# Kernel optimization log

Hardware: AMD Instinct MI355X
Metric: run time of the kernel (lower is better)

The kernel has to match this reference:

```python
import jax, jax.numpy as jnp
import numpy as np

B, FREQ, FRAMES = 16, 513, 2048
N_FFT, HOP, WIN = 1024, 256, 1024


def _hann_periodic(n):
    # torch.hann_window(n) (periodic): 0.5 - 0.5*cos(2*pi*k/n)
    return (0.5 - 0.5 * jnp.cos(2.0 * jnp.pi * jnp.arange(n) / n)).astype(jnp.float32)


def setup_inputs() -> dict:
    key = jax.random.key(0)
    k1, k2 = jax.random.split(key)
    spec_real = jax.random.normal(k1, (B, FREQ, FRAMES), dtype=jnp.float32)
    spec_imag = jax.random.normal(k2, (B, FREQ, FRAMES), dtype=jnp.float32)
    window = _hann_periodic(WIN)
    return {
        "spec_real": spec_real,
        "spec_imag": spec_imag,
        "window": window,
        "n_fft": N_FFT,
        "hop_length": HOP,
        "win_length": WIN,
    }


def reference(spec_real, spec_imag, window, n_fft, hop_length, win_length):
    spec = spec_real + 1j * spec_imag          # [B, n_fft//2+1, n_frames] complex
    n_frames = spec.shape[-1]
    pad = (win_length - hop_length) // 2
    # irfft with torch norm='backward' == jnp default norm
    ifft = jnp.fft.irfft(spec, n=n_fft, axis=1)           # [B, n_fft, F]
    frames = (ifft * window[None, :, None]).transpose(0, 2, 1)
    out_len = (n_frames - 1) * hop_length + win_length
    # overlap-add (fold) via scatter-add
    idx = jnp.arange(n_frames)[:, None] * hop_length + jnp.arange(win_length)[None, :]
    audio = jnp.zeros((frames.shape[0], out_len), frames.dtype).at[:, idx].add(frames)
    # squared-window envelope via the same overlap-add
    env = jnp.zeros((out_len,), window.dtype).at[idx].add(
        jnp.broadcast_to(window * window, (n_frames, win_length))
    )
    audio = audio[:, pad:out_len - pad] / env[pad:out_len - pad]
    return audio[:, None, :]  # [B, 1, T]
```

## Files before the change

### kernel.cpp

```cpp
#include <hip/hip_runtime.h>


#define B_      16
#define FREQ_   513
#define FRAMES_ 2048
#define NFFT_   1024
#define HOP_    256
#define NH_     512
#define PAD_    384
#define T_OUT_  524288
#define HPW     12
#define SPW     3072
#define NCHUNK  171

#define ZSTR2   513
#define XWSTR   513
#define TWF     16416
#define PREF    17440
#define LDSF    18464

__device__ __forceinline__ void idft8(float* zr, float* zi) {
  const float C = 0.70710678118654752f;
  float tr, ti;
  tr = zr[0]-zr[4]; ti = zi[0]-zi[4]; zr[0]+=zr[4]; zi[0]+=zi[4]; zr[4]=tr;         zi[4]=ti;
  tr = zr[1]-zr[5]; ti = zi[1]-zi[5]; zr[1]+=zr[5]; zi[1]+=zi[5]; zr[5]=C*(tr-ti);  zi[5]=C*(tr+ti);
  tr = zr[2]-zr[6]; ti = zi[2]-zi[6]; zr[2]+=zr[6]; zi[2]+=zi[6]; zr[6]=-ti;        zi[6]=tr;
  tr = zr[3]-zr[7]; ti = zi[3]-zi[7]; zr[3]+=zr[7]; zi[3]+=zi[7]; zr[7]=-C*(tr+ti); zi[7]=C*(tr-ti);
  tr = zr[0]-zr[2]; ti = zi[0]-zi[2]; zr[0]+=zr[2]; zi[0]+=zi[2]; zr[2]=tr;  zi[2]=ti;
  tr = zr[1]-zr[3]; ti = zi[1]-zi[3]; zr[1]+=zr[3]; zi[1]+=zi[3]; zr[3]=-ti; zi[3]=tr;
  tr = zr[4]-zr[6]; ti = zi[4]-zi[6]; zr[4]+=zr[6]; zi[4]+=zi[6]; zr[6]=tr;  zi[6]=ti;
  tr = zr[5]-zr[7]; ti = zi[5]-zi[7]; zr[5]+=zr[7]; zi[5]+=zi[7]; zr[7]=-ti; zi[7]=tr;
  tr = zr[0]-zr[1]; ti = zi[0]-zi[1]; zr[0]+=zr[1]; zi[0]+=zi[1]; zr[1]=tr; zi[1]=ti;
  tr = zr[2]-zr[3]; ti = zi[2]-zi[3]; zr[2]+=zr[3]; zi[2]+=zi[3]; zr[3]=tr; zi[3]=ti;
  tr = zr[4]-zr[5]; ti = zi[4]-zi[5]; zr[4]+=zr[5]; zi[4]+=zi[5]; zr[5]=tr; zi[5]=ti;
  tr = zr[6]-zr[7]; ti = zi[6]-zi[7]; zr[6]+=zr[7]; zi[6]+=zi[7]; zr[7]=tr; zi[7]=ti;
}

__global__ __launch_bounds__(1024, 8) void k_fused(
    const float* __restrict__ sre, const float* __restrict__ sim,
    const float* __restrict__ win, float* __restrict__ out) {
  __shared__ __align__(16) float lds[LDSF];
  float2* __restrict__ Z2  = (float2*)lds;
  float2* __restrict__ TW  = (float2*)(lds + TWF);
  float2* __restrict__ PRE = (float2*)(lds + PREF);

  const int t = threadIdx.x;
  const int f = t & 15;
  const int j = t >> 4;
  const int b   = blockIdx.x & 15;
  const int wgq = blockIdx.x >> 4;
  const int f_base = HPW * wgq - 2;
  const int s0     = SPW * wgq;
  const int fg = f_base + f;
  const bool fv = (fg >= 0) && (fg < FRAMES_);
  const int fgc = fv ? fg : 0;
  const float scale = fv ? (0.5f / 512.0f) : 0.0f;
  const size_t bbase = (size_t)b * (FREQ_ * FRAMES_);
  const float* __restrict__ srb = sre + bbase + fgc;
  const float* __restrict__ sib = sim + bbase + fgc;
  const int brev3[8] = {0, 4, 2, 6, 1, 5, 3, 7};

  float xr1[8], xi1[8], xr2[8], xi2[8];
#pragma unroll
  for (int m = 0; m < 8; ++m) {
    const int i  = j + (m << 6);
    const int k2 = NH_ - i;
    xr1[m] = srb[(size_t)i  * FRAMES_];
    xi1[m] = sib[(size_t)i  * FRAMES_];
    xr2[m] = srb[(size_t)k2 * FRAMES_];
    xi2[m] = sib[(size_t)k2 * FRAMES_];
  }

  {
    float s_, c_;
    if (t < 512) {
      sincosf((float)t * (6.2831853071795864769f / 512.f), &s_, &c_);
      TW[t] = make_float2(c_, s_);
    } else {
      const int k = t - 512;
      sincosf((float)k * (3.1415926535897932385f / 512.f), &s_, &c_);
      PRE[k] = make_float2(c_, s_);
    }
  }
  __syncthreads();

  {
    float zr[8], zi[8];
#pragma unroll
    for (int m = 0; m < 8; ++m) {
      const int i = j + (m << 6);
      float a  = xr1[m], bi_ = xi1[m];
      float cr = xr2[m], di  = xi2[m];
      if (i == 0) { bi_ = 0.f; di = 0.f; }
      const float Er = a + cr, Ei = bi_ - di;
      const float Dr = a - cr, Di = bi_ + di;
      const float2 w = PRE[i];
      const float Or = w.x * Dr - w.y * Di;
      const float Oi = w.x * Di + w.y * Dr;
      zr[m] = (Er - Oi) * scale;
      zi[m] = (Ei + Or) * scale;
    }
    idft8(zr, zi);
    float2* __restrict__ zrow = Z2 + f * ZSTR2 + j;
#pragma unroll
    for (int r = 0; r < 8; ++r) {
      const int mp = brev3[r];
      if (mp == 0) zrow[0] = make_float2(zr[r], zi[r]);
      else {
        const float2 w = TW[j * mp];
        zrow[mp << 6] = make_float2(zr[r] * w.x - zi[r] * w.y,
                                    zr[r] * w.y + zi[r] * w.x);
      }
    }
  }
  __syncthreads();

  {
    const int pos = j & 7, blk = j >> 3;
    float2* __restrict__ zrow = Z2 + f * ZSTR2 + (blk << 6) + pos;
    float zr[8], zi[8];
#pragma unroll
    for (int m = 0; m < 8; ++m) {
      const float2 v = zrow[m << 3];
      zr[m] = v.x; zi[m] = v.y;
    }
    idft8(zr, zi);
#pragma unroll
    for (int r = 0; r < 8; ++r) {
      const int mp = brev3[r];
      if (mp == 0) zrow[0] = make_float2(zr[r], zi[r]);
      else {
        const float2 w = TW[(pos * mp) << 3];
        zrow[mp << 3] = make_float2(zr[r] * w.x - zi[r] * w.y,
                                    zr[r] * w.y + zi[r] * w.x);
      }
    }
  }
  __syncthreads();

  float yr[8], yi[8];
  {
    const float2* __restrict__ zrow = Z2 + f * ZSTR2 + (j << 3);
#pragma unroll
    for (int m = 0; m < 8; ++m) {
      const float2 v = zrow[m];
      yr[m] = v.x; yi[m] = v.y;
    }
  }
  const int c = ((j & 7) << 3) + (j >> 3);
  float2 wv[8];
  {
    const float2* __restrict__ win2 = (const float2*)win;
#pragma unroll
    for (int r = 0; r < 8; ++r) wv[r] = win2[(brev3[r] << 6) + c];
  }
  idft8(yr, yi);
  __syncthreads();

  float* __restrict__ XWe = lds;
  float* __restrict__ XWo = lds + 16 * XWSTR;
  {
    float* __restrict__ er = XWe + f * XWSTR + c;
    float* __restrict__ od = XWo + f * XWSTR + c;
#pragma unroll
    for (int r = 0; r < 8; ++r) {
      const int mp = brev3[r];
      er[mp << 6] = yr[r] * wv[r].x;
      od[mp << 6] = yi[r] * wv[r].y;
    }
  }
  __syncthreads();

  float* __restrict__ outb = out + (size_t)b * T_OUT_;
#pragma unroll
  for (int rr = 0; rr < 2; ++rr) {
    const int idx = t + (rr << 10);
    if (idx < 1536) {
      const int s = s0 + (idx << 1);
      if (s < T_OUT_) {
        const int u   = s + PAD_;
        const int fh  = u >> 8;
        const int me0 = (u & 255) >> 1;
        float vr = 0.f, vi = 0.f;
#pragma unroll
        for (int jj = 0; jj < 4; ++jj) {
          const int fl = fh - jj - f_base;
          const int a  = fl * XWSTR + me0 + (jj << 7);
          vr += XWe[a]; vi += XWo[a];
        }
        float ivx, ivy;
        if (u >= 768 && u <= T_OUT_ - 2) {
          ivx = 0.66666666667f; ivy = 0.66666666667f;
        } else {
          float iv[2];
#pragma unroll
          for (int h = 0; h < 2; ++h) {
            const int uu  = u + h;
            const int fh2 = min(FRAMES_ - 1, uu >> 8);
            const int fl2 = (uu >= NFFT_) ? (((uu - NFFT_) >> 8) + 1) : 0;
            float e = 0.f;
            for (int ff = fl2; ff <= fh2; ++ff) {
              const float w = win[uu - (ff << 8)];
              e += w * w;
            }
            iv[h] = 1.0f / e;
          }
          ivx = iv[0]; ivy = iv[1];
        }
        *(float2*)(outb + s) = make_float2(vr * ivx, vi * ivy);
      }
    }
  }
}

extern "C" void kernel_launch(void* const* d_in, const int* in_sizes, int n_in,
                              void* d_out, int out_size, void* d_ws, size_t ws_size,
                              hipStream_t stream) {
  (void)in_sizes; (void)n_in; (void)out_size; (void)d_ws; (void)ws_size;
  const float* sre = (const float*)d_in[0];
  const float* sim = (const float*)d_in[1];
  const float* win = (const float*)d_in[2];
  float* out = (float*)d_out;
  k_fused<<<B_ * NCHUNK, 1024, 0, stream>>>(sre, sim, win, out);
}
```

Measured before the change: 202.5 us.

## Stage spectrum tile in LDS with coalesced loads and per-wave FFT rows

The spectrum is now loaded with float2-wide coalesced reads across frame pairs and transposed into LDS. Each 64-thread wave then owns one frame's row, so the FFT stages use XOR-swizzled LDS addressing and only an lgkmcnt wait instead of block-wide barriers. The window is cached in LDS and sincosf is swapped for __sincosf. This targets the strided global loads and the repeated __syncthreads. In exchange it relies on wave-local ordering of LDS accesses, and __sincosf gives slightly less accurate twiddles.

```diff
diff --git a/kernel.cpp b/kernel.cpp
--- a/kernel.cpp
+++ b/kernel.cpp
@@ -4,7 +4,6 @@
 #define B_      16
 #define FREQ_   513
 #define FRAMES_ 2048
-#define NFFT_   1024
 #define HOP_    256
 #define NH_     512
 #define PAD_    384
@@ -13,11 +12,13 @@
 #define SPW     3072
 #define NCHUNK  171
 
-#define ZSTR2   513
-#define XWSTR   513
-#define TWF     16416
-#define PREF    17440
-#define LDSF    18464
+#define FS2     515
+#define TWOFF   8240
+#define PREOFF  8752
+#define WINOFF  9264
+#define LDS2N   9776
+
+#define LGKM_SYNC() asm volatile("s_waitcnt lgkmcnt(0)" ::: "memory")
 
 __device__ __forceinline__ void idft8(float* zr, float* zi) {
   const float C = 0.70710678118654752f;
@@ -39,139 +40,144 @@
 __global__ __launch_bounds__(1024, 8) void k_fused(
     const float* __restrict__ sre, const float* __restrict__ sim,
     const float* __restrict__ win, float* __restrict__ out) {
-  __shared__ __align__(16) float lds[LDSF];
-  float2* __restrict__ Z2  = (float2*)lds;
-  float2* __restrict__ TW  = (float2*)(lds + TWF);
-  float2* __restrict__ PRE = (float2*)(lds + PREF);
-
-  const int t = threadIdx.x;
-  const int f = t & 15;
-  const int j = t >> 4;
+  __shared__ __align__(16) float2 lds2[LDS2N];
+  float2* S    = lds2;
+  float2* TW2  = lds2 + TWOFF;
+  float2* PRE2 = lds2 + PREOFF;
+  float2* WIN2 = lds2 + WINOFF;
+
+  const int t   = threadIdx.x;
   const int b   = blockIdx.x & 15;
   const int wgq = blockIdx.x >> 4;
   const int f_base = HPW * wgq - 2;
   const int s0     = SPW * wgq;
-  const int fg = f_base + f;
-  const bool fv = (fg >= 0) && (fg < FRAMES_);
-  const int fgc = fv ? fg : 0;
-  const float scale = fv ? (0.5f / 512.0f) : 0.0f;
-  const size_t bbase = (size_t)b * (FREQ_ * FRAMES_);
-  const float* __restrict__ srb = sre + bbase + fgc;
-  const float* __restrict__ sib = sim + bbase + fgc;
+
+  {
+    const float2* __restrict__ sre2 = (const float2*)sre + (size_t)b * (FREQ_ * 1024);
+    const float2* __restrict__ sim2 = (const float2*)sim + (size_t)b * (FREQ_ * 1024);
+    const int wp  = t & 7;
+    const int fg0 = f_base + (wp << 1);
+    const int cb2 = (min(max(fg0, 0), FRAMES_ - 2)) >> 1;
+    const int row0 = t >> 3;
+#pragma unroll
+    for (int k = 0; k < 4; ++k) {
+      const int row = row0 + (k << 7);
+      const int a   = (row << 10) + cb2;
+      const float2 re2 = sre2[a];
+      const float2 im2 = sim2[a];
+      S[(wp << 1) * FS2 + row]       = make_float2(re2.x, im2.x);
+      S[((wp << 1) + 1) * FS2 + row] = make_float2(re2.y, im2.y);
+    }
+    if (t < 8) {
+      const int a = (512 << 10) + cb2;
+      const float2 re2 = sre2[a];
+      const float2 im2 = sim2[a];
+      S[(wp << 1) * FS2 + 512]       = make_float2(re2.x, im2.x);
+      S[((wp << 1) + 1) * FS2 + 512] = make_float2(re2.y, im2.y);
+    }
+  }
+
+  if (t < 512) {
+    float s_, c_;
+    __sincosf((float)t * (6.2831853071795864769f / 512.f), &s_, &c_);
+    TW2[t]  = make_float2(c_, s_);
+    WIN2[t] = ((const float2*)win)[t];
+  } else {
+    const int k = t - 512;
+    float s_, c_;
+    __sincosf((float)k * (3.1415926535897932385f / 512.f), &s_, &c_);
+    PRE2[k] = make_float2(c_, s_);
+  }
+  __syncthreads();
+
+  const int w  = t >> 6;
+  const int j  = t & 63;
+  const int fg = f_base + w;
+  const float scale = (fg >= 0 && fg < FRAMES_) ? (0.5f / 512.0f) : 0.0f;
+  float2* Zs = S + w * FS2;
   const int brev3[8] = {0, 4, 2, 6, 1, 5, 3, 7};
 
-  float xr1[8], xi1[8], xr2[8], xi2[8];
+  float2 x1[8], x2[8];
 #pragma unroll
   for (int m = 0; m < 8; ++m) {
-    const int i  = j + (m << 6);
-    const int k2 = NH_ - i;
-    xr1[m] = srb[(size_t)i  * FRAMES_];
-    xi1[m] = sib[(size_t)i  * FRAMES_];
-    xr2[m] = srb[(size_t)k2 * FRAMES_];
-    xi2[m] = sib[(size_t)k2 * FRAMES_];
-  }
-
-  {
-    float s_, c_;
-    if (t < 512) {
-      sincosf((float)t * (6.2831853071795864769f / 512.f), &s_, &c_);
-      TW[t] = make_float2(c_, s_);
-    } else {
-      const int k = t - 512;
-      sincosf((float)k * (3.1415926535897932385f / 512.f), &s_, &c_);
-      PRE[k] = make_float2(c_, s_);
-    }
-  }
-  __syncthreads();
-
-  {
-    float zr[8], zi[8];
+    x1[m] = Zs[j + (m << 6)];
+    x2[m] = Zs[512 - j - (m << 6)];
+  }
+  float zr[8], zi[8];
+#pragma unroll
+  for (int m = 0; m < 8; ++m) {
+    const int i = j + (m << 6);
+    float ar = x1[m].x, ai = x1[m].y;
+    float br = x2[m].x, bi = x2[m].y;
+    if (i == 0) { ai = 0.f; bi = 0.f; }
+    const float Er = ar + br, Ei = ai - bi;
+    const float Dr = ar - br, Di = ai + bi;
+    const float2 pw = PRE2[i];
+    const float Or = pw.x * Dr - pw.y * Di;
+    const float Oi = pw.x * Di + pw.y * Dr;
+    zr[m] = (Er - Oi) * scale;
+    zi[m] = (Ei + Or) * scale;
+  }
+  idft8(zr, zi);
+  const int jx = j ^ (j >> 3);
+#pragma unroll
+  for (int r = 0; r < 8; ++r) {
+    const int mp = brev3[r];
+    const int a  = (mp << 6) | (jx ^ (mp << 3));
+    if (mp == 0) Zs[a] = make_float2(zr[r], zi[r]);
+    else {
+      const float2 tw = TW2[j * mp];
+      Zs[a] = make_float2(zr[r]*tw.x - zi[r]*tw.y, zr[r]*tw.y + zi[r]*tw.x);
+    }
+  }
+  LGKM_SYNC();
+  {
+    const int pos = j & 7, blk = j >> 3;
 #pragma unroll
     for (int m = 0; m < 8; ++m) {
-      const int i = j + (m << 6);
-      float a  = xr1[m], bi_ = xi1[m];
-      float cr = xr2[m], di  = xi2[m];
-      if (i == 0) { bi_ = 0.f; di = 0.f; }
-      const float Er = a + cr, Ei = bi_ - di;
-      const float Dr = a - cr, Di = bi_ + di;
-      const float2 w = PRE[i];
-      const float Or = w.x * Dr - w.y * Di;
-      const float Oi = w.x * Di + w.y * Dr;
-      zr[m] = (Er - Oi) * scale;
-      zi[m] = (Ei + Or) * scale;
+      const int a = (blk << 6) | (((m << 3) | pos) ^ ((blk << 3) | m));
+      const float2 v = Zs[a];
+      zr[m] = v.x; zi[m] = v.y;
     }
     idft8(zr, zi);
-    float2* __restrict__ zrow = Z2 + f * ZSTR2 + j;
 #pragma unroll
     for (int r = 0; r < 8; ++r) {
       const int mp = brev3[r];
-      if (mp == 0) zrow[0] = make_float2(zr[r], zi[r]);
+      const int a  = (blk << 6) | (((mp << 3) | pos) ^ ((blk << 3) | mp));
+      if (mp == 0) Zs[a] = make_float2(zr[r], zi[r]);
       else {
-        const float2 w = TW[j * mp];
-        zrow[mp << 6] = make_float2(zr[r] * w.x - zi[r] * w.y,
-                                    zr[r] * w.y + zi[r] * w.x);
+        const float2 tw = TW2[(pos * mp) << 3];
+        Zs[a] = make_float2(zr[r]*tw.x - zi[r]*tw.y, zr[r]*tw.y + zi[r]*tw.x);
       }
     }
   }
-  __syncthreads();
-
-  {
-    const int pos = j & 7, blk = j >> 3;
-    float2* __restrict__ zrow = Z2 + f * ZSTR2 + (blk << 6) + pos;
-    float zr[8], zi[8];
+  LGKM_SYNC();
+  float yr[8], yi[8];
+  {
+    const int b3 = (j << 3) ^ j;
 #pragma unroll
     for (int m = 0; m < 8; ++m) {
-      const float2 v = zrow[m << 3];
-      zr[m] = v.x; zi[m] = v.y;
-    }
-    idft8(zr, zi);
+      const float2 v = Zs[b3 ^ m];
+      yr[m] = v.x; yi[m] = v.y;
+    }
+  }
+  idft8(yr, yi);
+  {
+    const int c = ((j & 7) << 3) | (j >> 3);
+    float* XWrow = (float*)Zs;
 #pragma unroll
     for (int r = 0; r < 8; ++r) {
       const int mp = brev3[r];
-      if (mp == 0) zrow[0] = make_float2(zr[r], zi[r]);
-      else {
-        const float2 w = TW[(pos * mp) << 3];
-        zrow[mp << 3] = make_float2(zr[r] * w.x - zi[r] * w.y,
-                                    zr[r] * w.y + zi[r] * w.x);
-      }
+      const int mt = (mp << 6) | c;
+      const float2 wv = WIN2[mt];
+      XWrow[mt]       = yr[r] * wv.x;
+      XWrow[512 + mt] = yi[r] * wv.y;
     }
   }
   __syncthreads();
 
-  float yr[8], yi[8];
-  {
-    const float2* __restrict__ zrow = Z2 + f * ZSTR2 + (j << 3);
-#pragma unroll
-    for (int m = 0; m < 8; ++m) {
-      const float2 v = zrow[m];
-      yr[m] = v.x; yi[m] = v.y;
-    }
-  }
-  const int c = ((j & 7) << 3) + (j >> 3);
-  float2 wv[8];
-  {
-    const float2* __restrict__ win2 = (const float2*)win;
-#pragma unroll
-    for (int r = 0; r < 8; ++r) wv[r] = win2[(brev3[r] << 6) + c];
-  }
-  idft8(yr, yi);
-  __syncthreads();
-
-  float* __restrict__ XWe = lds;
-  float* __restrict__ XWo = lds + 16 * XWSTR;
-  {
-    float* __restrict__ er = XWe + f * XWSTR + c;
-    float* __restrict__ od = XWo + f * XWSTR + c;
-#pragma unroll
-    for (int r = 0; r < 8; ++r) {
-      const int mp = brev3[r];
-      er[mp << 6] = yr[r] * wv[r].x;
-      od[mp << 6] = yi[r] * wv[r].y;
-    }
-  }
-  __syncthreads();
-
   float* __restrict__ outb = out + (size_t)b * T_OUT_;
+  const float* ldsf = (const float*)lds2;
 #pragma unroll
   for (int rr = 0; rr < 2; ++rr) {
     const int idx = t + (rr << 10);
@@ -185,8 +191,9 @@
 #pragma unroll
         for (int jj = 0; jj < 4; ++jj) {
           const int fl = fh - jj - f_base;
-          const int a  = fl * XWSTR + me0 + (jj << 7);
-          vr += XWe[a]; vi += XWo[a];
+          const int af = fl * (FS2 * 2) + (jj << 7) + me0;
+          vr += ldsf[af];
+          vi += ldsf[af + 512];
         }
         float ivx, ivy;
         if (u >= 768 && u <= T_OUT_ - 2) {
@@ -197,11 +204,11 @@
           for (int h = 0; h < 2; ++h) {
             const int uu  = u + h;
             const int fh2 = min(FRAMES_ - 1, uu >> 8);
-            const int fl2 = (uu >= NFFT_) ? (((uu - NFFT_) >> 8) + 1) : 0;
+            const int fl2 = (uu >= 1024) ? (((uu - 1024) >> 8) + 1) : 0;
             float e = 0.f;
             for (int ff = fl2; ff <= fh2; ++ff) {
-              const float w = win[uu - (ff << 8)];
-              e += w * w;
+              const float ww = win[uu - (ff << 8)];
+              e += ww * ww;
             }
             iv[h] = 1.0f / e;
           }
```

Result: faster. 189.3 us (-6.5%).
